# Performance work log

Hardware: AMD Instinct MI355X
Metric: run time of the kernel (lower is better)

## Reference

```python
import jax, jax.numpy as jnp
import numpy as np

N = 8192
D = 1024
TIME_DECAY = 86400.0
EPS = 1e-10


def setup_inputs() -> dict:
    key = jax.random.key(0)
    ks = jax.random.split(key, 8)
    x = jax.random.normal(ks[0], (N, D), dtype=jnp.float32)
    # timestamps spanning ~10 days so decay bias is non-trivial
    timestamps = jax.random.uniform(ks[1], (N,), dtype=jnp.float32) * (10.0 * TIME_DECAY)
    s = 1.0 / np.sqrt(D)
    Wq = jax.random.normal(ks[2], (D, D), dtype=jnp.float32) * s
    bq = jnp.zeros((D,), dtype=jnp.float32)
    Wk = jax.random.normal(ks[3], (D, D), dtype=jnp.float32) * s
    bk = jnp.zeros((D,), dtype=jnp.float32)
    Wv = jax.random.normal(ks[4], (D, D), dtype=jnp.float32) * s
    bv = jnp.zeros((D,), dtype=jnp.float32)
    return {"x": x, "timestamps": timestamps, "Wq": Wq, "bq": bq,
            "Wk": Wk, "bk": bk, "Wv": Wv, "bv": bv}


def reference(x, timestamps, Wq, bq, Wk, bk, Wv, bv):
    scale = jnp.asarray(D ** 0.5, x.dtype)
    # torch nn.Linear: y = x @ W.T + b
    Q = x @ Wq.T + bq          # [N, D]
    K = x @ Wk.T + bk          # [N, D]
    V = x @ Wv.T + bv          # [N, D]
    time_diff = timestamps[:, None] - timestamps[None, :]   # [N, N]
    time_decay = jnp.exp(-jnp.abs(time_diff) / TIME_DECAY)  # [N, N]
    scores = (Q @ K.T) / scale + jnp.log(time_decay + EPS)  # [N, N]
    attn = jax.nn.softmax(scores, axis=-1)
    return attn @ V
```

## Files before the change

kernel.cpp:

```cpp
#include <hip/hip_runtime.h>


using half8   = __attribute__((ext_vector_type(8))) _Float16;
using half4   = __attribute__((ext_vector_type(4))) _Float16;
using floatx4 = __attribute__((ext_vector_type(4))) float;

__device__ __forceinline__ void gload_lds16(const void* g, void* l) {
  __builtin_amdgcn_global_load_lds((const __attribute__((address_space(1))) void*)g,
                                   (__attribute__((address_space(3))) void*)l,
                                   16, 0, 0);
}

template<int N> __device__ __forceinline__ void waitv() {
  if constexpr (N == 6) asm volatile("s_waitcnt vmcnt(6)" ::: "memory");
  else                  asm volatile("s_waitcnt vmcnt(0)" ::: "memory");
}
__device__ __forceinline__ void waitl0() {
  asm volatile("s_waitcnt lgkmcnt(0)");
}

template<int MI, int NJ>
__device__ __forceinline__ void kloop_c(
    const _Float16* __restrict__ A, const _Float16* __restrict__ B,
    long rowBase, long colBase, int lda, int ldb, int K,
    _Float16* __restrict__ As, _Float16* __restrict__ Bs,
    floatx4 (&acc)[MI][NJ])
{
  static_assert(MI == 8 && NJ == 4);
  const int tid = threadIdx.x;
  const int w = tid >> 6, lane = tid & 63;
  const int q = lane >> 4, l15 = lane & 15;
  const int wr = w >> 2, wcn = w & 3;

  const int sc = ((lane & 7) ^ (lane >> 3)) << 3;
  const _Float16* Agp[4]; const _Float16* Bgp[4];
#pragma unroll
  for (int p = 0; p < 4; ++p) {
    Agp[p] = A + (rowBase + p * 64 + (tid >> 3)) * (long)lda + sc;
    Bgp[p] = B + (colBase + p * 64 + (tid >> 3)) * (long)ldb + sc;
  }
  const int ldsOff = tid * 8;

  const int aRow = wr * 128 + l15;
  const int bRow = wcn * 64 + l15;
  const int cx = l15 & 7;
  const int pc0 = (q ^ cx) << 3, pc1 = ((4 + q) ^ cx) << 3;

  auto stageA = [&](int t, int h) {
    _Float16* dst = As + (t & 1) * (256 * 64);
    const int ko = t << 6;
#pragma unroll
    for (int p = 2 * h; p < 2 * h + 2; ++p)
      gload_lds16(Agp[p] + ko, dst + p * 4096 + ldsOff);
  };
  auto stageB = [&](int t, int h, int slot) {
    _Float16* dst = Bs + slot * (256 * 64);
    const int ko = t << 6;
#pragma unroll
    for (int p = 2 * h; p < 2 * h + 2; ++p)
      gload_lds16(Bgp[p] + ko, dst + p * 4096 + ldsOff);
  };

  const int NT = K >> 6;
  stageB(0, 0, 0); stageB(0, 1, 0); stageA(0, 0); stageA(0, 1);
  stageB(1, 0, 1); stageB(1, 1, 1); stageA(1, 0);
  waitv<6>(); __builtin_amdgcn_s_barrier();

  int bs_ = 0;
  for (int t = 0; t < NT; ++t) {
    const _Float16* Asl = As + (t & 1) * (256 * 64);
    const _Float16* Bsl = Bs + bs_ * (256 * 64);
    const int bs2 = (bs_ == 0) ? 2 : bs_ - 1;
    half8 b0[NJ], b1[NJ], a0lo[MI / 2], a0hi[MI / 2], a1[MI];

#pragma unroll
    for (int j = 0; j < NJ; ++j)
      b0[j] = *(const half8*)&Bsl[(bRow + 16 * j) * 64 + pc0];
#pragma unroll
    for (int i = 0; i < MI / 2; ++i)
      a0lo[i] = *(const half8*)&Asl[(aRow + 16 * i) * 64 + pc0];
    if (t + 1 < NT) stageA(t + 1, 1);
    __builtin_amdgcn_s_barrier();
    waitl0();
    __builtin_amdgcn_s_setprio(1);
#pragma unroll
    for (int i = 0; i < MI / 2; ++i)
#pragma unroll
      for (int j = 0; j < NJ; ++j)
        acc[i][j] = __builtin_amdgcn_mfma_f32_16x16x32_f16(a0lo[i], b0[j], acc[i][j], 0, 0, 0);
    __builtin_amdgcn_s_setprio(0);
    __builtin_amdgcn_s_barrier();

#pragma unroll
    for (int i = 0; i < MI / 2; ++i)
      a0hi[i] = *(const half8*)&Asl[(aRow + 16 * (MI / 2 + i)) * 64 + pc0];
#pragma unroll
    for (int j = 0; j < NJ; ++j)
      b1[j] = *(const half8*)&Bsl[(bRow + 16 * j) * 64 + pc1];
    if (t + 2 < NT) stageB(t + 2, 0, bs2);
    __builtin_amdgcn_s_barrier();
    waitl0();
    __builtin_amdgcn_s_setprio(1);
#pragma unroll
    for (int i = 0; i < MI / 2; ++i)
#pragma unroll
      for (int j = 0; j < NJ; ++j)
        acc[MI / 2 + i][j] = __builtin_amdgcn_mfma_f32_16x16x32_f16(a0hi[i], b0[j], acc[MI / 2 + i][j], 0, 0, 0);
    __builtin_amdgcn_s_setprio(0);
    __builtin_amdgcn_s_barrier();

#pragma unroll
    for (int i = 0; i < MI; ++i)
      a1[i] = *(const half8*)&Asl[(aRow + 16 * i) * 64 + pc1];
    if (t + 2 < NT) stageB(t + 2, 1, bs2);
    __builtin_amdgcn_s_barrier();
    waitl0();
    __builtin_amdgcn_s_setprio(1);
#pragma unroll
    for (int i = 0; i < MI / 2; ++i)
#pragma unroll
      for (int j = 0; j < NJ; ++j)
        acc[i][j] = __builtin_amdgcn_mfma_f32_16x16x32_f16(a1[i], b1[j], acc[i][j], 0, 0, 0);
    __builtin_amdgcn_s_setprio(0);
    __builtin_amdgcn_s_barrier();

    if (t + 2 < NT) stageA(t + 2, 0);
    __builtin_amdgcn_s_barrier();
    __builtin_amdgcn_s_setprio(1);
#pragma unroll
    for (int i = 0; i < MI / 2; ++i)
#pragma unroll
      for (int j = 0; j < NJ; ++j)
        acc[MI / 2 + i][j] = __builtin_amdgcn_mfma_f32_16x16x32_f16(a1[MI / 2 + i], b1[j], acc[MI / 2 + i][j], 0, 0, 0);
    __builtin_amdgcn_s_setprio(0);
    if (t < NT - 2)       { waitv<6>(); __builtin_amdgcn_s_barrier(); }
    else if (t == NT - 2) { waitv<0>(); __builtin_amdgcn_s_barrier(); }
    bs_ = (bs_ == 2) ? 0 : bs_ + 1;
  }
}

template<int BM, int BN, int WM, int WN, int SLOTS, int PH, int MI, int NJ>
__device__ __forceinline__ void kloop_f(
    const _Float16* __restrict__ A, const _Float16* __restrict__ B,
    long rowBase, long colBase, int lda, int ldb, int K,
    _Float16* __restrict__ As, _Float16* __restrict__ Bs,
    floatx4 (&acc)[MI][NJ])
{
  static_assert(MI == BM / WM / 16 && NJ == BN / WN / 16 && MI % PH == 0);
  constexpr int LA = BM / 64, LB = BN / 64;
  constexpr int RP = MI / PH;
  const int tid = threadIdx.x;
  const int w = tid >> 6, lane = tid & 63;
  const int q = lane >> 4, l15 = lane & 15;
  const int wr = w / WN, wcn = w & (WN - 1);

  const int sc = ((lane & 7) ^ (lane >> 3)) << 3;
  const _Float16* Agp[LA]; const _Float16* Bgp[LB];
#pragma unroll
  for (int p = 0; p < LA; ++p)
    Agp[p] = A + (rowBase + p * 64 + (tid >> 3)) * (long)lda + sc;
#pragma unroll
  for (int p = 0; p < LB; ++p)
    Bgp[p] = B + (colBase + p * 64 + (tid >> 3)) * (long)ldb + sc;
  const int ldsOff = tid * 8;

  const int aRow = wr * (BM / WM) + l15;
  const int bRow = wcn * (BN / WN) + l15;
  const int cx = l15 & 7;

  auto issueA = [&](int t, int s) {
    _Float16* Asl = As + s * (BM * 64);
    const int ko = t << 6;
#pragma unroll
    for (int p = 0; p < LA; ++p) gload_lds16(Agp[p] + ko, Asl + p * 4096 + ldsOff);
  };
  auto issueB = [&](int t, int s) {
    _Float16* Bsl = Bs + s * (BN * 64);
    const int ko = t << 6;
#pragma unroll
    for (int p = 0; p < LB; ++p) gload_lds16(Bgp[p] + ko, Bsl + p * 4096 + ldsOff);
  };

  half8 bfr[2][NJ];

  auto tile = [&](int t, int slot, bool doStage, int ew) {
    const _Float16* Asl = As + slot * (BM * 64);
    const _Float16* Bsl = Bs + slot * (BN * 64);
    const int st = t + SLOTS - 1;
    const int ss = (SLOTS == 2) ? (slot ^ 1) : (st % 3);
#pragma unroll
    for (int ph = 0; ph < PH; ++ph) {
      half8 afr[2][RP];
      if (ph == 0) {
#pragma unroll
        for (int kk = 0; kk < 2; ++kk) {
          const int pc = ((kk * 4 + q) ^ cx) << 3;
#pragma unroll
          for (int j = 0; j < NJ; ++j)
            bfr[kk][j] = *(const half8*)&Bsl[(bRow + 16 * j) * 64 + pc];
        }
      }
#pragma unroll
      for (int kk = 0; kk < 2; ++kk) {
        const int pc = ((kk * 4 + q) ^ cx) << 3;
#pragma unroll
        for (int r = 0; r < RP; ++r)
          afr[kk][r] = *(const half8*)&Asl[(aRow + 16 * (ph * RP + r)) * 64 + pc];
      }
      if (doStage && ph == 0) issueA(st, ss);
      if (doStage && ph == 1) issueB(st, ss);
      __builtin_amdgcn_s_barrier();
      waitl0();
      __builtin_amdgcn_s_setprio(1);
#pragma unroll
      for (int kk = 0; kk < 2; ++kk)
#pragma unroll
        for (int r = 0; r < RP; ++r)
#pragma unroll
          for (int j = 0; j < NJ; ++j)
            acc[ph * RP + r][j] = __builtin_amdgcn_mfma_f32_16x16x32_f16(
                afr[kk][r], bfr[kk][j], acc[ph * RP + r][j], 0, 0, 0);
      __builtin_amdgcn_s_setprio(0);
      if (ph == PH - 1) {
        if (ew == 6)      waitv<6>();
        else if (ew == 0) waitv<0>();
        if (ew >= 0) __builtin_amdgcn_s_barrier();
      } else {
        __builtin_amdgcn_s_barrier();
      }
    }
  };

  const int NT = K >> 6;
  static_assert(SLOTS == 3);
  issueA(0, 0); issueB(0, 0);
  issueA(1, 1); issueB(1, 1);
  waitv<6>(); __builtin_amdgcn_s_barrier();
  int cs = 0;
  for (int t = 0; t < NT - 1; ++t) {
    const bool st = (t + 2 < NT);
    tile(t, cs, st, (t < NT - 2) ? 6 : 0);
    cs = (cs == 2) ? 0 : cs + 1;
  }
  tile(NT - 1, cs, false, -1);
}

template<int BM, int BN, int WM, int WN, int SLOTS, int PH,
         int BIAS_MODE, int OUT_MODE, int SWZ>
__global__ __launch_bounds__(512, 2)
void gemm256_k(const _Float16* __restrict__ A, const _Float16* __restrict__ B,
               void* __restrict__ Cout, const float* __restrict__ bias,
               int lda, int ldb, int ldc, int K, float outScale)
{
  constexpr int MI = BM / WM / 16, NJ = BN / WN / 16;
  __shared__ __align__(16) _Float16 As[SLOTS * BM * 64];
  __shared__ __align__(16) _Float16 Bs[SLOTS * BN * 64];

  int tx, ty;
  if (SWZ) {
    const int bflat = blockIdx.y * gridDim.x + blockIdx.x;
    ty = bflat % gridDim.y;
    tx = bflat / gridDim.y;
  } else {
    tx = blockIdx.x; ty = blockIdx.y;
  }
  const long rowBase = (long)ty * BM;
  const long colBase = (long)tx * BN;

  floatx4 acc[MI][NJ] = {};
  kloop_f<BM, BN, WM, WN, SLOTS, PH, MI, NJ>(A, B, rowBase, colBase, lda, ldb, K,
                                             As, Bs, acc);

  const int tid = threadIdx.x;
  const int w = tid >> 6, lane = tid & 63;
  const int q = lane >> 4, l15 = lane & 15;
  const int wr = w / WN, wcn = w & (WN - 1);
#pragma unroll
  for (int i = 0; i < MI; ++i) {
#pragma unroll
    for (int r = 0; r < 4; ++r) {
      const long rowg = rowBase + wr * (BM / WM) + 16 * i + q * 4 + r;
#pragma unroll
      for (int j = 0; j < NJ; ++j) {
        const long colg = colBase + wcn * (BN / WN) + 16 * j + l15;
        float v = acc[i][j][r];
        if (BIAS_MODE == 1) v += bias[colg];
        if (BIAS_MODE == 2) v += bias[rowg];
        if (BIAS_MODE == 3) v *= bias[rowg];
        v *= outScale;
        if (OUT_MODE == 2) ((float*)Cout)[rowg * ldc + colg] = v;
        else               ((_Float16*)Cout)[rowg * ldc + colg] = (_Float16)v;
      }
    }
  }
}

template<int BIAS_MODE, int OUT_MODE>
__global__ __launch_bounds__(512, 2)
void gemm256c_k(const _Float16* __restrict__ A, const _Float16* __restrict__ B,
                void* __restrict__ Cout, const float* __restrict__ bias,
                int lda, int ldb, int ldc, int K, float outScale)
{
  __shared__ __align__(16) _Float16 As[2 * 256 * 64];
  __shared__ __align__(16) _Float16 Bs[3 * 256 * 64];
  const long rowBase = (long)blockIdx.y * 256;
  const long colBase = (long)blockIdx.x * 256;

  floatx4 acc[8][4] = {};
  kloop_c<8, 4>(A, B, rowBase, colBase, lda, ldb, K, As, Bs, acc);

  const int tid = threadIdx.x;
  const int w = tid >> 6, lane = tid & 63;
  const int q = lane >> 4, l15 = lane & 15;
  const int wr = w >> 2, wcn = w & 3;
#pragma unroll
  for (int i = 0; i < 8; ++i) {
#pragma unroll
    for (int r = 0; r < 4; ++r) {
      const long rowg = rowBase + wr * 128 + 16 * i + q * 4 + r;
#pragma unroll
      for (int j = 0; j < 4; ++j) {
        const long colg = colBase + wcn * 64 + 16 * j + l15;
        float v = acc[i][j][r];
        if (BIAS_MODE == 1) v += bias[colg];
        if (BIAS_MODE == 2) v += bias[rowg];
        v *= outScale;
        if (OUT_MODE == 2) ((float*)Cout)[rowg * ldc + colg] = v;
        else               ((_Float16*)Cout)[rowg * ldc + colg] = (_Float16)v;
      }
    }
  }
}

__global__ __launch_bounds__(512, 2)
void gemm_statsC_k(const _Float16* __restrict__ A, const _Float16* __restrict__ B,
                   const float* __restrict__ ts, _Float16* __restrict__ U,
                   float* __restrict__ part, int lda, int ldb, int N, int K,
                   float qkScale)
{
  __shared__ __align__(16) _Float16 As[2 * 256 * 64];
  __shared__ __align__(16) _Float16 Bs[3 * 256 * 64];
  const int tid = threadIdx.x;
  const long rowBase = (long)blockIdx.y * 256;
  const long colBase = (long)blockIdx.x * 256;

  floatx4 acc[8][4] = {};
  kloop_c<8, 4>(A, B, rowBase, colBase, lda, ldb, K, As, Bs, acc);

  const int w = tid >> 6, lane = tid & 63;
  const int q = lane >> 4, l15 = lane & 15;
  const int wr = w >> 2, wcn = w & 3;
  const float inv_td = 1.0f / 86400.0f;

  float tc[4];
#pragma unroll
  for (int j = 0; j < 4; ++j) tc[j] = ts[colBase + wcn * 64 + 16 * j + l15];

  float* sl = (float*)As;
  __syncthreads();
#pragma unroll
  for (int i = 0; i < 8; ++i) {
#pragma unroll
    for (int r = 0; r < 4; ++r) {
      const int rowl = wr * 128 + 16 * i + q * 4 + r;
      const float tr = ts[rowBase + rowl];
      float ls = 0.0f;
#pragma unroll
      for (int j = 0; j < 4; ++j) {
        const int coll = wcn * 64 + 16 * j + l15;
        const float sv = acc[i][j][r] * qkScale
                       - fabsf(tr - tc[j]) * inv_td - 4.0f;
        const float u = __expf(sv);
        ls += u;
        U[(rowBase + rowl) * (long)N + (colBase + coll)] = (_Float16)u;
      }
      for (int mask = 1; mask <= 8; mask <<= 1)
        ls += __shfl_xor(ls, mask, 64);
      if (l15 == 0) sl[(wr * 4 + wcn) * 128 + 16 * i + 4 * q + r] = ls;
    }
  }
  __syncthreads();
  if (tid < 256) {
    const int band = tid & 127, hi = tid >> 7;
    part[(rowBase + tid) * 32 + blockIdx.x] =
        sl[(hi * 4 + 0) * 128 + band] + sl[(hi * 4 + 1) * 128 + band] +
        sl[(hi * 4 + 2) * 128 + band] + sl[(hi * 4 + 3) * 128 + band];
  }
}

__global__ void combine_k(const float* __restrict__ part, float* __restrict__ invL) {
  const int r = blockIdx.x * 256 + threadIdx.x;
  float L = 0.0f;
  for (int c = 0; c < 32; ++c) L += part[(long)r * 32 + c];
  invL[r] = 1.0f / L;
}

__global__ void cvt_k(const float* __restrict__ in, _Float16* __restrict__ out, int n) {
  const int i = (blockIdx.x * 256 + threadIdx.x) * 4;
  if (i >= n) return;
  const float4 v = *(const float4*)(in + i);
  half4 o = { (_Float16)v.x, (_Float16)v.y, (_Float16)v.z, (_Float16)v.w };
  *(half4*)(out + i) = o;
}

extern "C" void kernel_launch(void* const* d_in, const int* in_sizes, int n_in,
                              void* d_out, int out_size, void* d_ws, size_t ws_size,
                              hipStream_t stream)
{
  (void)in_sizes; (void)n_in; (void)out_size; (void)ws_size;
  const int N = 8192, D = 1024;
  const float* x  = (const float*)d_in[0];
  const float* ts = (const float*)d_in[1];
  const float* Wq = (const float*)d_in[2];
  const float* bq = (const float*)d_in[3];
  const float* Wk = (const float*)d_in[4];
  const float* bk = (const float*)d_in[5];
  const float* Wv = (const float*)d_in[6];
  const float* bv = (const float*)d_in[7];

  char* p = (char*)d_ws;
  auto grab = [&](size_t bytes) {
    char* r = p;
    p += (bytes + 255) & ~(size_t)255;
    return r;
  };
  _Float16* xh    = (_Float16*)grab((size_t)N * D * 2);
  _Float16* wqkh  = (_Float16*)grab((size_t)2 * D * D * 2);
  _Float16* wvh   = (_Float16*)grab((size_t)D * D * 2);
  _Float16* QKcat = (_Float16*)grab((size_t)N * 2 * D * 2);
  _Float16* VTh   = (_Float16*)grab((size_t)D * N * 2);
  _Float16* Uh    = (_Float16*)grab((size_t)N * N * 2);
  float*    part  = (float*)grab((size_t)N * 32 * sizeof(float));
  float*    invL  = (float*)grab((size_t)N * sizeof(float));
  float*    bcat  = (float*)grab((size_t)2 * D * sizeof(float));

  cvt_k<<<N * D / 1024, 256, 0, stream>>>(x,  xh,  N * D);
  cvt_k<<<D * D / 1024, 256, 0, stream>>>(Wq, wqkh,         D * D);
  cvt_k<<<D * D / 1024, 256, 0, stream>>>(Wk, wqkh + D * D, D * D);
  cvt_k<<<D * D / 1024, 256, 0, stream>>>(Wv, wvh, D * D);
  hipMemcpyAsync(bcat,     bq, D * sizeof(float), hipMemcpyDeviceToDevice, stream);
  hipMemcpyAsync(bcat + D, bk, D * sizeof(float), hipMemcpyDeviceToDevice, stream);

  dim3 blk(512);
  gemm256c_k<1, 0><<<dim3(2 * D / 256, N / 256), blk, 0, stream>>>(
      xh, wqkh, QKcat, bcat, D, D, 2 * D, D, 1.0f);
  gemm256_k<256, 128, 4, 2, 3, 2, 2, 0, 0><<<dim3(N / 128, D / 256), blk, 0, stream>>>(
      wvh, xh, VTh, bv, D, D, N, D, 1.0f);
  gemm_statsC_k<<<dim3(N / 256, N / 256), blk, 0, stream>>>(
      QKcat, QKcat + D, ts, Uh, part, 2 * D, 2 * D, N, D, 1.0f / 32.0f);
  combine_k<<<N / 256, 256, 0, stream>>>(part, invL);
  gemm256_k<256, 128, 4, 2, 3, 2, 3, 2, 1><<<dim3(D / 128, N / 256), blk, 0, stream>>>(
      Uh, VTh, d_out, invL, N, N, D, N, 1.0f);
}
```

Baseline: 500.4 us.

## Simplify GEMM main loops to one barrier per K-tile with fewer sync phases

```diff
diff --git a/kernel.cpp b/kernel.cpp
--- a/kernel.cpp
+++ b/kernel.cpp
@@ -12,21 +12,25 @@
 }
 
 template<int N> __device__ __forceinline__ void waitv() {
-  if constexpr (N == 6) asm volatile("s_waitcnt vmcnt(6)" ::: "memory");
-  else                  asm volatile("s_waitcnt vmcnt(0)" ::: "memory");
-}
-__device__ __forceinline__ void waitl0() {
-  asm volatile("s_waitcnt lgkmcnt(0)");
-}
-
-template<int MI, int NJ>
-__device__ __forceinline__ void kloop_c(
+  if constexpr (N == 8)      asm volatile("s_waitcnt vmcnt(8)" ::: "memory");
+  else if constexpr (N == 6) asm volatile("s_waitcnt vmcnt(6)" ::: "memory");
+  else                       asm volatile("s_waitcnt vmcnt(0)" ::: "memory");
+}
+
+#define MFMA16(ar, br, accrow)                                              \
+  _Pragma("unroll")                                                         \
+  for (int i_ = 0; i_ < 4; ++i_)                                            \
+    _Pragma("unroll")                                                       \
+    for (int j_ = 0; j_ < 4; ++j_)                                          \
+      accrow[i_][j_] = __builtin_amdgcn_mfma_f32_16x16x32_f16(              \
+          ar[i_], br[j_], accrow[i_][j_], 0, 0, 0);
+
+__device__ __forceinline__ void kloop_s(
     const _Float16* __restrict__ A, const _Float16* __restrict__ B,
     long rowBase, long colBase, int lda, int ldb, int K,
     _Float16* __restrict__ As, _Float16* __restrict__ Bs,
-    floatx4 (&acc)[MI][NJ])
-{
-  static_assert(MI == 8 && NJ == 4);
+    floatx4 (&acc)[8][4])
+{
   const int tid = threadIdx.x;
   const int w = tid >> 6, lane = tid & 63;
   const int q = lane >> 4, l15 = lane & 15;
@@ -46,268 +50,144 @@
   const int cx = l15 & 7;
   const int pc0 = (q ^ cx) << 3, pc1 = ((4 + q) ^ cx) << 3;
 
-  auto stageA = [&](int t, int h) {
-    _Float16* dst = As + (t & 1) * (256 * 64);
+  auto stageA = [&](int t) {
+    _Float16* dst = As + (t & 1) * 16384;
     const int ko = t << 6;
 #pragma unroll
-    for (int p = 2 * h; p < 2 * h + 2; ++p)
-      gload_lds16(Agp[p] + ko, dst + p * 4096 + ldsOff);
+    for (int p = 0; p < 4; ++p) gload_lds16(Agp[p] + ko, dst + p * 4096 + ldsOff);
   };
-  auto stageB = [&](int t, int h, int slot) {
-    _Float16* dst = Bs + slot * (256 * 64);
+  auto stageB = [&](int t) {
+    _Float16* dst = Bs + (t & 1) * 16384;
     const int ko = t << 6;
 #pragma unroll
-    for (int p = 2 * h; p < 2 * h + 2; ++p)
-      gload_lds16(Bgp[p] + ko, dst + p * 4096 + ldsOff);
+    for (int p = 0; p < 4; ++p) gload_lds16(Bgp[p] + ko, dst + p * 4096 + ldsOff);
   };
 
   const int NT = K >> 6;
-  stageB(0, 0, 0); stageB(0, 1, 0); stageA(0, 0); stageA(0, 1);
-  stageB(1, 0, 1); stageB(1, 1, 1); stageA(1, 0);
-  waitv<6>(); __builtin_amdgcn_s_barrier();
-
-  int bs_ = 0;
+  stageA(0); stageB(0); stageA(1); stageB(1);
+  waitv<8>(); __builtin_amdgcn_s_barrier();
+
   for (int t = 0; t < NT; ++t) {
-    const _Float16* Asl = As + (t & 1) * (256 * 64);
-    const _Float16* Bsl = Bs + bs_ * (256 * 64);
-    const int bs2 = (bs_ == 0) ? 2 : bs_ - 1;
-    half8 b0[NJ], b1[NJ], a0lo[MI / 2], a0hi[MI / 2], a1[MI];
-
-#pragma unroll
-    for (int j = 0; j < NJ; ++j)
-      b0[j] = *(const half8*)&Bsl[(bRow + 16 * j) * 64 + pc0];
-#pragma unroll
-    for (int i = 0; i < MI / 2; ++i)
-      a0lo[i] = *(const half8*)&Asl[(aRow + 16 * i) * 64 + pc0];
-    if (t + 1 < NT) stageA(t + 1, 1);
+    const _Float16* Asl = As + (t & 1) * 16384;
+    const _Float16* Bsl = Bs + (t & 1) * 16384;
+    half8 b0[4], b1[4], a0lo[4], a0hi[4], a1lo[4], a1hi[4];
+
+#pragma unroll
+    for (int j = 0; j < 4; ++j) b0[j]   = *(const half8*)&Bsl[(bRow + 16 * j) * 64 + pc0];
+#pragma unroll
+    for (int i = 0; i < 4; ++i) a0lo[i] = *(const half8*)&Asl[(aRow + 16 * i) * 64 + pc0];
+#pragma unroll
+    for (int i = 0; i < 4; ++i) a0hi[i] = *(const half8*)&Asl[(aRow + 16 * (4 + i)) * 64 + pc0];
+    {
+      floatx4 (&alo)[4][4] = *(floatx4(*)[4][4])&acc[0];
+      MFMA16(a0lo, b0, alo);
+    }
+#pragma unroll
+    for (int j = 0; j < 4; ++j) b1[j]   = *(const half8*)&Bsl[(bRow + 16 * j) * 64 + pc1];
+#pragma unroll
+    for (int i = 0; i < 4; ++i) a1lo[i] = *(const half8*)&Asl[(aRow + 16 * i) * 64 + pc1];
+    {
+      floatx4 (&ahi)[4][4] = *(floatx4(*)[4][4])&acc[4];
+      MFMA16(a0hi, b0, ahi);
+    }
+#pragma unroll
+    for (int i = 0; i < 4; ++i) a1hi[i] = *(const half8*)&Asl[(aRow + 16 * (4 + i)) * 64 + pc1];
+    {
+      floatx4 (&alo)[4][4] = *(floatx4(*)[4][4])&acc[0];
+      MFMA16(a1lo, b1, alo);
+    }
+
+    asm volatile("s_waitcnt lgkmcnt(0)" ::: "memory");
     __builtin_amdgcn_s_barrier();
-    waitl0();
-    __builtin_amdgcn_s_setprio(1);
-#pragma unroll
-    for (int i = 0; i < MI / 2; ++i)
-#pragma unroll
-      for (int j = 0; j < NJ; ++j)
-        acc[i][j] = __builtin_amdgcn_mfma_f32_16x16x32_f16(a0lo[i], b0[j], acc[i][j], 0, 0, 0);
-    __builtin_amdgcn_s_setprio(0);
-    __builtin_amdgcn_s_barrier();
-
-#pragma unroll
-    for (int i = 0; i < MI / 2; ++i)
-      a0hi[i] = *(const half8*)&Asl[(aRow + 16 * (MI / 2 + i)) * 64 + pc0];
-#pragma unroll
-    for (int j = 0; j < NJ; ++j)
-      b1[j] = *(const half8*)&Bsl[(bRow + 16 * j) * 64 + pc1];
-    if (t + 2 < NT) stageB(t + 2, 0, bs2);
-    __builtin_amdgcn_s_barrier();
-    waitl0();
-    __builtin_amdgcn_s_setprio(1);
-#pragma unroll
-    for (int i = 0; i < MI / 2; ++i)
-#pragma unroll
-      for (int j = 0; j < NJ; ++j)
-        acc[MI / 2 + i][j] = __builtin_amdgcn_mfma_f32_16x16x32_f16(a0hi[i], b0[j], acc[MI / 2 + i][j], 0, 0, 0);
-    __builtin_amdgcn_s_setprio(0);
-    __builtin_amdgcn_s_barrier();
-
-#pragma unroll
-    for (int i = 0; i < MI; ++i)
-      a1[i] = *(const half8*)&Asl[(aRow + 16 * i) * 64 + pc1];
-    if (t + 2 < NT) stageB(t + 2, 1, bs2);
-    __builtin_amdgcn_s_barrier();
-    waitl0();
-    __builtin_amdgcn_s_setprio(1);
-#pragma unroll
-    for (int i = 0; i < MI / 2; ++i)
-#pragma unroll
-      for (int j = 0; j < NJ; ++j)
-        acc[i][j] = __builtin_amdgcn_mfma_f32_16x16x32_f16(a1[i], b1[j], acc[i][j], 0, 0, 0);
-    __builtin_amdgcn_s_setprio(0);
-    __builtin_amdgcn_s_barrier();
-
-    if (t + 2 < NT) stageA(t + 2, 0);
-    __builtin_amdgcn_s_barrier();
-    __builtin_amdgcn_s_setprio(1);
-#pragma unroll
-    for (int i = 0; i < MI / 2; ++i)
-#pragma unroll
-      for (int j = 0; j < NJ; ++j)
-        acc[MI / 2 + i][j] = __builtin_amdgcn_mfma_f32_16x16x32_f16(a1[MI / 2 + i], b1[j], acc[MI / 2 + i][j], 0, 0, 0);
-    __builtin_amdgcn_s_setprio(0);
-    if (t < NT - 2)       { waitv<6>(); __builtin_amdgcn_s_barrier(); }
-    else if (t == NT - 2) { waitv<0>(); __builtin_amdgcn_s_barrier(); }
-    bs_ = (bs_ == 2) ? 0 : bs_ + 1;
-  }
-}
-
-template<int BM, int BN, int WM, int WN, int SLOTS, int PH, int MI, int NJ>
-__device__ __forceinline__ void kloop_f(
+    if (t + 2 < NT) { stageA(t + 2); stageB(t + 2); }
+    {
+      floatx4 (&ahi)[4][4] = *(floatx4(*)[4][4])&acc[4];
+      MFMA16(a1hi, b1, ahi);
+    }
+    if (t < NT - 1) {
+      if (t + 2 < NT) waitv<8>(); else waitv<0>();
+      __builtin_amdgcn_s_barrier();
+    }
+  }
+}
+
+__device__ __forceinline__ void kloop_v(
     const _Float16* __restrict__ A, const _Float16* __restrict__ B,
     long rowBase, long colBase, int lda, int ldb, int K,
     _Float16* __restrict__ As, _Float16* __restrict__ Bs,
-    floatx4 (&acc)[MI][NJ])
-{
-  static_assert(MI == BM / WM / 16 && NJ == BN / WN / 16 && MI % PH == 0);
-  constexpr int LA = BM / 64, LB = BN / 64;
-  constexpr int RP = MI / PH;
-  const int tid = threadIdx.x;
-  const int w = tid >> 6, lane = tid & 63;
-  const int q = lane >> 4, l15 = lane & 15;
-  const int wr = w / WN, wcn = w & (WN - 1);
+    floatx4 (&acc)[4][4])
+{
+  const int tid = threadIdx.x;
+  const int w = tid >> 6, lane = tid & 63;
+  const int q = lane >> 4, l15 = lane & 15;
+  const int wr = w >> 1, wcn = w & 1;
 
   const int sc = ((lane & 7) ^ (lane >> 3)) << 3;
-  const _Float16* Agp[LA]; const _Float16* Bgp[LB];
-#pragma unroll
-  for (int p = 0; p < LA; ++p)
+  const _Float16* Agp[4]; const _Float16* Bgp[2];
+#pragma unroll
+  for (int p = 0; p < 4; ++p)
     Agp[p] = A + (rowBase + p * 64 + (tid >> 3)) * (long)lda + sc;
 #pragma unroll
-  for (int p = 0; p < LB; ++p)
+  for (int p = 0; p < 2; ++p)
     Bgp[p] = B + (colBase + p * 64 + (tid >> 3)) * (long)ldb + sc;
   const int ldsOff = tid * 8;
 
-  const int aRow = wr * (BM / WM) + l15;
-  const int bRow = wcn * (BN / WN) + l15;
+  const int aRow = wr * 64 + l15;
+  const int bRow = wcn * 64 + l15;
   const int cx = l15 & 7;
-
-  auto issueA = [&](int t, int s) {
-    _Float16* Asl = As + s * (BM * 64);
+  const int pc0 = (q ^ cx) << 3, pc1 = ((4 + q) ^ cx) << 3;
+
+  auto stage = [&](int t) {
+    const int s = t % 3;
+    _Float16* dA = As + s * 16384;
+    _Float16* dB = Bs + s * 8192;
     const int ko = t << 6;
 #pragma unroll
-    for (int p = 0; p < LA; ++p) gload_lds16(Agp[p] + ko, Asl + p * 4096 + ldsOff);
+    for (int p = 0; p < 4; ++p) gload_lds16(Agp[p] + ko, dA + p * 4096 + ldsOff);
+#pragma unroll
+    for (int p = 0; p < 2; ++p) gload_lds16(Bgp[p] + ko, dB + p * 4096 + ldsOff);
   };
-  auto issueB = [&](int t, int s) {
-    _Float16* Bsl = Bs + s * (BN * 64);
-    const int ko = t << 6;
-#pragma unroll
-    for (int p = 0; p < LB; ++p) gload_lds16(Bgp[p] + ko, Bsl + p * 4096 + ldsOff);
-  };
-
-  half8 bfr[2][NJ];
-
-  auto tile = [&](int t, int slot, bool doStage, int ew) {
-    const _Float16* Asl = As + slot * (BM * 64);
-    const _Float16* Bsl = Bs + slot * (BN * 64);
-    const int st = t + SLOTS - 1;
-    const int ss = (SLOTS == 2) ? (slot ^ 1) : (st % 3);
-#pragma unroll
-    for (int ph = 0; ph < PH; ++ph) {
-      half8 afr[2][RP];
-      if (ph == 0) {
-#pragma unroll
-        for (int kk = 0; kk < 2; ++kk) {
-          const int pc = ((kk * 4 + q) ^ cx) << 3;
-#pragma unroll
-          for (int j = 0; j < NJ; ++j)
-            bfr[kk][j] = *(const half8*)&Bsl[(bRow + 16 * j) * 64 + pc];
-        }
-      }
-#pragma unroll
-      for (int kk = 0; kk < 2; ++kk) {
-        const int pc = ((kk * 4 + q) ^ cx) << 3;
-#pragma unroll
-        for (int r = 0; r < RP; ++r)
-          afr[kk][r] = *(const half8*)&Asl[(aRow + 16 * (ph * RP + r)) * 64 + pc];
-      }
-      if (doStage && ph == 0) issueA(st, ss);
-      if (doStage && ph == 1) issueB(st, ss);
+
+  const int NT = K >> 6;
+  stage(0); stage(1);
+  waitv<6>(); __builtin_amdgcn_s_barrier();
+
+  for (int t = 0; t < NT; ++t) {
+    const int s = t % 3;
+    const _Float16* Asl = As + s * 16384;
+    const _Float16* Bsl = Bs + s * 8192;
+    half8 b0[4], b1[4], a0[4], a1[4];
+#pragma unroll
+    for (int j = 0; j < 4; ++j) b0[j] = *(const half8*)&Bsl[(bRow + 16 * j) * 64 + pc0];
+#pragma unroll
+    for (int i = 0; i < 4; ++i) a0[i] = *(const half8*)&Asl[(aRow + 16 * i) * 64 + pc0];
+#pragma unroll
+    for (int j = 0; j < 4; ++j) b1[j] = *(const half8*)&Bsl[(bRow + 16 * j) * 64 + pc1];
+#pragma unroll
+    for (int i = 0; i < 4; ++i) a1[i] = *(const half8*)&Asl[(aRow + 16 * i) * 64 + pc1];
+    MFMA16(a0, b0, acc);
+    if (t + 2 < NT) stage(t + 2);
+    MFMA16(a1, b1, acc);
+    if (t < NT - 1) {
+      if (t + 2 < NT) waitv<6>(); else waitv<0>();
       __builtin_amdgcn_s_barrier();
-      waitl0();
-      __builtin_amdgcn_s_setprio(1);
-#pragma unroll
-      for (int kk = 0; kk < 2; ++kk)
-#pragma unroll
-        for (int r = 0; r < RP; ++r)
-#pragma unroll
-          for (int j = 0; j < NJ; ++j)
-            acc[ph * RP + r][j] = __builtin_amdgcn_mfma_f32_16x16x32_f16(
-                afr[kk][r], bfr[kk][j], acc[ph * RP + r][j], 0, 0, 0);
-      __builtin_amdgcn_s_setprio(0);
-      if (ph == PH - 1) {
-        if (ew == 6)      waitv<6>();
-        else if (ew == 0) waitv<0>();
-        if (ew >= 0) __builtin_amdgcn_s_barrier();
-      } else {
-        __builtin_amdgcn_s_barrier();
-      }
-    }
-  };
-
-  const int NT = K >> 6;
-  static_assert(SLOTS == 3);
-  issueA(0, 0); issueB(0, 0);
-  issueA(1, 1); issueB(1, 1);
-  waitv<6>(); __builtin_amdgcn_s_barrier();
-  int cs = 0;
-  for (int t = 0; t < NT - 1; ++t) {
-    const bool st = (t + 2 < NT);
-    tile(t, cs, st, (t < NT - 2) ? 6 : 0);
-    cs = (cs == 2) ? 0 : cs + 1;
-  }
-  tile(NT - 1, cs, false, -1);
-}
-
-template<int BM, int BN, int WM, int WN, int SLOTS, int PH,
-         int BIAS_MODE, int OUT_MODE, int SWZ>
-__global__ __launch_bounds__(512, 2)
-void gemm256_k(const _Float16* __restrict__ A, const _Float16* __restrict__ B,
-               void* __restrict__ Cout, const float* __restrict__ bias,
-               int lda, int ldb, int ldc, int K, float outScale)
-{
-  constexpr int MI = BM / WM / 16, NJ = BN / WN / 16;
-  __shared__ __align__(16) _Float16 As[SLOTS * BM * 64];
-  __shared__ __align__(16) _Float16 Bs[SLOTS * BN * 64];
-
-  int tx, ty;
-  if (SWZ) {
-    const int bflat = blockIdx.y * gridDim.x + blockIdx.x;
-    ty = bflat % gridDim.y;
-    tx = bflat / gridDim.y;
-  } else {
-    tx = blockIdx.x; ty = blockIdx.y;
-  }
-  const long rowBase = (long)ty * BM;
-  const long colBase = (long)tx * BN;
-
-  floatx4 acc[MI][NJ] = {};
-  kloop_f<BM, BN, WM, WN, SLOTS, PH, MI, NJ>(A, B, rowBase, colBase, lda, ldb, K,
-                                             As, Bs, acc);
-
-  const int tid = threadIdx.x;
-  const int w = tid >> 6, lane = tid & 63;
-  const int q = lane >> 4, l15 = lane & 15;
-  const int wr = w / WN, wcn = w & (WN - 1);
-#pragma unroll
-  for (int i = 0; i < MI; ++i) {
-#pragma unroll
-    for (int r = 0; r < 4; ++r) {
-      const long rowg = rowBase + wr * (BM / WM) + 16 * i + q * 4 + r;
-#pragma unroll
-      for (int j = 0; j < NJ; ++j) {
-        const long colg = colBase + wcn * (BN / WN) + 16 * j + l15;
-        float v = acc[i][j][r];
-        if (BIAS_MODE == 1) v += bias[colg];
-        if (BIAS_MODE == 2) v += bias[rowg];
-        if (BIAS_MODE == 3) v *= bias[rowg];
-        v *= outScale;
-        if (OUT_MODE == 2) ((float*)Cout)[rowg * ldc + colg] = v;
-        else               ((_Float16*)Cout)[rowg * ldc + colg] = (_Float16)v;
-      }
     }
   }
 }
 
 template<int BIAS_MODE, int OUT_MODE>
 __global__ __launch_bounds__(512, 2)
-void gemm256c_k(const _Float16* __restrict__ A, const _Float16* __restrict__ B,
-                void* __restrict__ Cout, const float* __restrict__ bias,
-                int lda, int ldb, int ldc, int K, float outScale)
-{
-  __shared__ __align__(16) _Float16 As[2 * 256 * 64];
-  __shared__ __align__(16) _Float16 Bs[3 * 256 * 64];
+void gemmS_k(const _Float16* __restrict__ A, const _Float16* __restrict__ B,
+             void* __restrict__ Cout, const float* __restrict__ bias,
+             int lda, int ldb, int ldc, int K, float outScale)
+{
+  __shared__ __align__(16) _Float16 As[2 * 16384];
+  __shared__ __align__(16) _Float16 Bs[2 * 16384];
   const long rowBase = (long)blockIdx.y * 256;
   const long colBase = (long)blockIdx.x * 256;
 
   floatx4 acc[8][4] = {};
-  kloop_c<8, 4>(A, B, rowBase, colBase, lda, ldb, K, As, Bs, acc);
+  kloop_s(A, B, rowBase, colBase, lda, ldb, K, As, Bs, acc);
 
   const int tid = threadIdx.x;
   const int w = tid >> 6, lane = tid & 63;
@@ -332,20 +212,67 @@
   }
 }
 
+template<int BIAS_MODE, int OUT_MODE, int SWZ>
 __global__ __launch_bounds__(512, 2)
-void gemm_statsC_k(const _Float16* __restrict__ A, const _Float16* __restrict__ B,
+void gemmV_k(const _Float16* __restrict__ A, const _Float16* __restrict__ B,
+             void* __restrict__ Cout, const float* __restrict__ bias,
+             int lda, int ldb, int ldc, int K, float outScale)
+{
+  __shared__ __align__(16) _Float16 As[3 * 16384];
+  __shared__ __align__(16) _Float16 Bs[3 * 8192];
+
+  int tx, ty;
+  if (SWZ) {
+    const int bflat = blockIdx.y * gridDim.x + blockIdx.x;
+    ty = bflat % gridDim.y;
+    tx = bflat / gridDim.y;
+  } else {
+    tx = blockIdx.x; ty = blockIdx.y;
+  }
+  const long rowBase = (long)ty * 256;
+  const long colBase = (long)tx * 128;
+
+  floatx4 acc[4][4] = {};
+  kloop_v(A, B, rowBase, colBase, lda, ldb, K, As, Bs, acc);
+
+  const int tid = threadIdx.x;
+  const int w = tid >> 6, lane = tid & 63;
+  const int q = lane >> 4, l15 = lane & 15;
+  const int wr = w >> 1, wcn = w & 1;
+#pragma unroll
+  for (int i = 0; i < 4; ++i) {
+#pragma unroll
+    for (int r = 0; r < 4; ++r) {
+      const long rowg = rowBase + wr * 64 + 16 * i + q * 4 + r;
+#pragma unroll
+      for (int j = 0; j < 4; ++j) {
+        const long colg = colBase + wcn * 64 + 16 * j + l15;
+        float v = acc[i][j][r];
+        if (BIAS_MODE == 1) v += bias[colg];
+        if (BIAS_MODE == 2) v += bias[rowg];
+        if (BIAS_MODE == 3) v *= bias[rowg];
+        v *= outScale;
+        if (OUT_MODE == 2) ((float*)Cout)[rowg * ldc + colg] = v;
+        else               ((_Float16*)Cout)[rowg * ldc + colg] = (_Float16)v;
+      }
+    }
+  }
+}
+
+__global__ __launch_bounds__(512, 2)
+void gemm_statsS_k(const _Float16* __restrict__ A, const _Float16* __restrict__ B,
                    const float* __restrict__ ts, _Float16* __restrict__ U,
                    float* __restrict__ part, int lda, int ldb, int N, int K,
                    float qkScale)
 {
-  __shared__ __align__(16) _Float16 As[2 * 256 * 64];
-  __shared__ __align__(16) _Float16 Bs[3 * 256 * 64];
+  __shared__ __align__(16) _Float16 As[2 * 16384];
+  __shared__ __align__(16) _Float16 Bs[2 * 16384];
   const int tid = threadIdx.x;
   const long rowBase = (long)blockIdx.y * 256;
   const long colBase = (long)blockIdx.x * 256;
 
   floatx4 acc[8][4] = {};
-  kloop_c<8, 4>(A, B, rowBase, colBase, lda, ldb, K, As, Bs, acc);
+  kloop_s(A, B, rowBase, colBase, lda, ldb, K, As, Bs, acc);
 
   const int w = tid >> 6, lane = tid & 63;
   const int q = lane >> 4, l15 = lane & 15;
@@ -442,13 +369,13 @@
   hipMemcpyAsync(bcat + D, bk, D * sizeof(float), hipMemcpyDeviceToDevice, stream);
 
   dim3 blk(512);
-  gemm256c_k<1, 0><<<dim3(2 * D / 256, N / 256), blk, 0, stream>>>(
+  gemmS_k<1, 0><<<dim3(2 * D / 256, N / 256), blk, 0, stream>>>(
       xh, wqkh, QKcat, bcat, D, D, 2 * D, D, 1.0f);
-  gemm256_k<256, 128, 4, 2, 3, 2, 2, 0, 0><<<dim3(N / 128, D / 256), blk, 0, stream>>>(
+  gemmV_k<2, 0, 0><<<dim3(N / 128, D / 256), blk, 0, stream>>>(
       wvh, xh, VTh, bv, D, D, N, D, 1.0f);
-  gemm_statsC_k<<<dim3(N / 256, N / 256), blk, 0, stream>>>(
+  gemm_statsS_k<<<dim3(N / 256, N / 256), blk, 0, stream>>>(
       QKcat, QKcat + D, ts, Uh, part, 2 * D, 2 * D, N, D, 1.0f / 32.0f);
   combine_k<<<N / 256, 256, 0, stream>>>(part, invL);
-  gemm256_k<256, 128, 4, 2, 3, 2, 3, 2, 1><<<dim3(D / 128, N / 256), blk, 0, stream>>>(
+  gemmV_k<3, 2, 1><<<dim3(D / 128, N / 256), blk, 0, stream>>>(
       Uh, VTh, d_out, invL, N, N, D, N, 1.0f);
 }
```

Measured after the change: 464.3 us. 7.2% less time.
